# Performance work log

Hardware: AMD Instinct MI355X
Metric: run time of the kernel (lower is better)

The kernel has to match this reference:

```python
import jax, jax.numpy as jnp
import numpy as np

V, I_DIM, H_DIM, NUM_CLASSES = 32000, 300, 300, 3
B, T = 64, 128


def setup_inputs() -> dict:
    key = jax.random.key(0)
    ks = jax.random.split(key, 32)
    def g(k, shape, s=0.05):
        return (jax.random.normal(k, shape, jnp.float32) * s)
    linputs = jax.random.randint(ks[0], (B, T), 0, V)
    rinputs = jax.random.randint(ks[1], (B, T), 0, V)
    # strictly-lower-triangular binary child masks (children processed before parents)
    tril = jnp.tril(jnp.ones((T, T), jnp.float32), k=-1)
    lgraph = (jax.random.uniform(ks[2], (B, T, T)) < 0.05).astype(jnp.float32) * tril
    rgraph = (jax.random.uniform(ks[3], (B, T, T)) < 0.05).astype(jnp.float32) * tril
    emb = g(ks[4], (V, I_DIM), 0.02).at[0].set(0.0)  # padding_idx=0
    names = ['wi', 'wf', 'wo', 'wu', 'ui', 'uf', 'uo', 'uu']
    params = {}
    for n, (kw, kb) in zip(names, [(ks[5 + 2 * i], ks[6 + 2 * i]) for i in range(8)]):
        params[n + '_w'] = g(kw, (H_DIM, I_DIM if n[0] == 'w' else H_DIM))
        params[n + '_b'] = g(kb, (H_DIM,))
    params['gcn_w'] = g(ks[21], (H_DIM, H_DIM))
    params['wh_w'] = g(ks[22], (H_DIM, 4 * H_DIM))
    params['wh_b'] = g(ks[23], (H_DIM,))
    params['wp_w'] = g(ks[24], (NUM_CLASSES, H_DIM))
    params['wp_b'] = g(ks[25], (NUM_CLASSES,))
    return dict(linputs=linputs, lgraph=lgraph, rinputs=rinputs, rgraph=rgraph, emb=emb, **params)


def _lin(x, w, b):
    return x @ w.T + b


def _forward(linputs, lgraph, rinputs, rgraph, emb,
             wi_w, wi_b, wf_w, wf_b, wo_w, wo_b, wu_w, wu_b,
             ui_w, ui_b, uf_w, uf_b, uo_w, uo_b, uu_w, uu_b,
             gcn_w, wh_w, wh_b, wp_w, wp_b):
    def tree_lstm(x, graph):
        Bd, Td, _ = x.shape
        # precompute input projections for all timesteps: [B,T,H]
        Xi = _lin(x, wi_w, wi_b)
        Xf = _lin(x, wf_w, wf_b)
        Xo = _lin(x, wo_w, wo_b)
        Xu = _lin(x, wu_w, wu_b)
        h0 = jnp.zeros((Bd, Td, H_DIM), x.dtype)
        c0 = jnp.zeros_like(h0)

        def step(carry, inp):
            h, c = carry
            xi, xf, xo, xu, mrow, j = inp  # xi..xu: [B,H], mrow: [B,T]
            hj = h[:, j]  # [B,H]
            i = jax.nn.sigmoid(xi + _lin(hj, ui_w, ui_b))
            o = jax.nn.sigmoid(xo + _lin(hj, uo_w, uo_b))
            u = jnp.tanh(xu + _lin(hj, uu_w, uu_b))
            f = jax.nn.sigmoid(xf[:, None, :] + _lin(h, uf_w, uf_b))  # [B,T,H]
            c_new = i * u + jnp.einsum('bt,bth->bh', mrow, f * c)
            h_new = o * jnp.tanh(c_new)
            return (h.at[:, j].set(h_new), c.at[:, j].set(c_new)), None

        xs = (jnp.swapaxes(Xi, 0, 1), jnp.swapaxes(Xf, 0, 1),
              jnp.swapaxes(Xo, 0, 1), jnp.swapaxes(Xu, 0, 1),
              jnp.swapaxes(graph, 0, 1), jnp.arange(Td))
        (h, c), _ = jax.lax.scan(step, (h0, c0), xs)
        return h, c

    def gcn(graph, h):
        Td = graph.shape[1]
        A = jnp.eye(Td, dtype=graph.dtype)[None] + jnp.swapaxes(graph, 1, 2) + graph
        return jax.nn.relu(jnp.einsum('bst,bth->bsh', A, h @ gcn_w))

    le = emb[linputs]
    re = emb[rinputs]
    lh, _ = tree_lstm(le, lgraph)
    rh, _ = tree_lstm(re, rgraph)
    ls = gcn(lgraph, lh)
    rs = gcn(rgraph, rh)
    v = jnp.concatenate([ls.max(axis=1), rs.max(axis=1), ls.mean(axis=1), rs.mean(axis=1)], axis=1)
    return _lin(jax.nn.relu(_lin(v, wh_w, wh_b)), wp_w, wp_b)


def reference(linputs, lgraph, rinputs, rgraph, emb,
              wi_w, wi_b, wf_w, wf_b, wo_w, wo_b, wu_w, wu_b,
              ui_w, ui_b, uf_w, uf_b, uo_w, uo_b, uu_w, uu_b,
              gcn_w, wh_w, wh_b, wp_w, wp_b):
    return _forward(linputs, lgraph, rinputs, rgraph, emb,
                    wi_w, wi_b, wf_w, wf_b, wo_w, wo_b, wu_w, wu_b,
                    ui_w, ui_b, uf_w, uf_b, uo_w, uo_b, uu_w, uu_b,
                    gcn_w, wh_w, wh_b, wp_w, wp_b)
```

## Files before the change

### kernel.cpp

```cpp
#include <hip/hip_runtime.h>
#include <math.h>

#define BD 64
#define TD 128
#define HD 300
#define NROW (2*BD*TD)
#define ROWSZ ((size_t)NROW*HD)
#define CMAX 32
#define AMAX 64

__device__ __forceinline__ float sigf(float x){ return 1.f/(1.f+expf(-x)); }

__global__ __launch_bounds__(256) void gates_gemm_k(
    const int* __restrict__ tokL, const int* __restrict__ tokR,
    const float* __restrict__ emb,
    const float* __restrict__ wi_w, const float* __restrict__ wf_w,
    const float* __restrict__ wo_w, const float* __restrict__ wu_w,
    const float* __restrict__ wi_b, const float* __restrict__ ui_b,
    const float* __restrict__ wf_b, const float* __restrict__ uf_b,
    const float* __restrict__ wo_b, const float* __restrict__ uo_b,
    const float* __restrict__ wu_b, const float* __restrict__ uu_b,
    float* __restrict__ IU, float* __restrict__ Og, float* __restrict__ F0)
{
  __shared__ __align__(16) float As[32][64];
  __shared__ __align__(16) float Bs[4][32][64];
  const int r0 = blockIdx.x * 64;
  const int n0 = blockIdx.y * 64;
  const int tid = threadIdx.x;

  const int am  = tid >> 2;
  const int akq = tid & 3;
  const float* arow;
  {
    int r = r0 + am;
    int tree = r >> 13;
    int tok  = (tree ? tokR : tokL)[r & 8191];
    arow = emb + (size_t)tok * HD;
  }

  const float* Bm[4] = {wi_w, wf_w, wo_w, wu_w};
  const int bn  = tid >> 2;
  const int bkq = tid & 3;
  const bool nok = (n0 + bn) < HD;

  const int tm = tid >> 4;
  const int tn = tid & 15;
  float acc[4][4][4] = {};

  for (int k0 = 0; k0 < HD; k0 += 32){
    #pragma unroll
    for (int h = 0; h < 2; ++h){
      int k  = akq*8 + h*4;
      int kg = k0 + k;
      float4 v;
      if (kg + 3 < HD) v = *(const float4*)(arow + kg);
      else {
        v.x = (kg   < HD) ? arow[kg]   : 0.f;
        v.y = (kg+1 < HD) ? arow[kg+1] : 0.f;
        v.z = (kg+2 < HD) ? arow[kg+2] : 0.f;
        v.w = (kg+3 < HD) ? arow[kg+3] : 0.f;
      }
      As[k+0][am] = v.x; As[k+1][am] = v.y; As[k+2][am] = v.z; As[k+3][am] = v.w;
    }
    #pragma unroll
    for (int g = 0; g < 4; ++g){
      const float* brow = Bm[g] + (size_t)(n0 + bn) * HD;
      #pragma unroll
      for (int h = 0; h < 2; ++h){
        int k  = bkq*8 + h*4;
        int kg = k0 + k;
        float4 v = {0.f,0.f,0.f,0.f};
        if (nok){
          if (kg + 3 < HD) v = *(const float4*)(brow + kg);
          else {
            if (kg   < HD) v.x = brow[kg];
            if (kg+1 < HD) v.y = brow[kg+1];
            if (kg+2 < HD) v.z = brow[kg+2];
          }
        }
        Bs[g][k+0][bn] = v.x; Bs[g][k+1][bn] = v.y;
        Bs[g][k+2][bn] = v.z; Bs[g][k+3][bn] = v.w;
      }
    }
    __syncthreads();

    #pragma unroll 8
    for (int k = 0; k < 32; ++k){
      float a[4];
      *(float4*)a = *(const float4*)&As[k][tm*4];
      #pragma unroll
      for (int g = 0; g < 4; ++g){
        float bb[4];
        *(float4*)bb = *(const float4*)&Bs[g][k][tn*4];
        #pragma unroll
        for (int i = 0; i < 4; ++i)
          #pragma unroll
          for (int j = 0; j < 4; ++j)
            acc[g][i][j] += a[i]*bb[j];
      }
    }
    __syncthreads();
  }

  #pragma unroll
  for (int j = 0; j < 4; ++j){
    int col = n0 + tn*4 + j;
    if (col >= HD) continue;
    float bi = wi_b[col] + ui_b[col];
    float bf = wf_b[col] + uf_b[col];
    float bo = wo_b[col] + uo_b[col];
    float bu = wu_b[col] + uu_b[col];
    #pragma unroll
    for (int i = 0; i < 4; ++i){
      int r = r0 + tm*4 + i;
      size_t idx = (size_t)r * HD + col;
      float ii = sigf(acc[0][i][j] + bi);
      float uu = tanhf(acc[3][i][j] + bu);
      IU[idx] = ii * uu;
      Og[idx] = sigf(acc[2][i][j] + bo);
      F0[idx] = acc[1][i][j] + bf;
    }
  }
}

__global__ __launch_bounds__(256) void gemm_nn_k(
    const float* __restrict__ A, const float* __restrict__ B,
    float* __restrict__ C)
{
  __shared__ __align__(16) float As[32][64];
  __shared__ __align__(16) float Bs[32][64];
  const int r0 = blockIdx.x * 64;
  const int n0 = blockIdx.y * 64;
  const int tid = threadIdx.x;

  const int am  = tid >> 2;
  const int akq = tid & 3;
  const float* arow = A + (size_t)(r0 + am) * HD;

  const int tm = tid >> 4;
  const int tn = tid & 15;
  float acc[4][4] = {};

  for (int k0 = 0; k0 < HD; k0 += 32){
    #pragma unroll
    for (int h = 0; h < 2; ++h){
      int k  = akq*8 + h*4;
      int kg = k0 + k;
      float4 v;
      if (kg + 3 < HD) v = *(const float4*)(arow + kg);
      else {
        v.x = (kg   < HD) ? arow[kg]   : 0.f;
        v.y = (kg+1 < HD) ? arow[kg+1] : 0.f;
        v.z = (kg+2 < HD) ? arow[kg+2] : 0.f;
        v.w = (kg+3 < HD) ? arow[kg+3] : 0.f;
      }
      As[k+0][am] = v.x; As[k+1][am] = v.y; As[k+2][am] = v.z; As[k+3][am] = v.w;
    }
    {
      int bk  = tid >> 3;
      int bnq = tid & 7;
      int kg  = k0 + bk;
      const float* brow = B + (size_t)kg * HD;
      #pragma unroll
      for (int h = 0; h < 2; ++h){
        int n  = bnq*8 + h*4;
        int ng = n0 + n;
        float4 v = {0.f,0.f,0.f,0.f};
        if (kg < HD){
          if (ng + 3 < HD) v = *(const float4*)(brow + ng);
          else {
            if (ng   < HD) v.x = brow[ng];
            if (ng+1 < HD) v.y = brow[ng+1];
            if (ng+2 < HD) v.z = brow[ng+2];
          }
        }
        *(float4*)&Bs[bk][n] = v;
      }
    }
    __syncthreads();

    #pragma unroll 8
    for (int k = 0; k < 32; ++k){
      float a[4], bb[4];
      *(float4*)a  = *(const float4*)&As[k][tm*4];
      *(float4*)bb = *(const float4*)&Bs[k][tn*4];
      #pragma unroll
      for (int i = 0; i < 4; ++i)
        #pragma unroll
        for (int j = 0; j < 4; ++j)
          acc[i][j] += a[i]*bb[j];
    }
    __syncthreads();
  }

  #pragma unroll
  for (int i = 0; i < 4; ++i){
    int r = r0 + tm*4 + i;
    #pragma unroll
    for (int j = 0; j < 4; ++j){
      int col = n0 + tn*4 + j;
      if (col < HD) C[(size_t)r * HD + col] = acc[i][j];
    }
  }
}

__global__ __launch_bounds__(320) void recurrence_k(
    float* IU_C,
    float* Og_H,
    float* F0_G,
    const float* __restrict__ gL, const float* __restrict__ gR,
    const float* __restrict__ ufw)
{
  const int wg   = blockIdx.x;
  const int tree = wg >> 6;
  const int b    = wg & 63;
  const float* graph = tree ? gR : gL;
  const int tid = threadIdx.x;

  __shared__ float  cw  [TD][CMAX];
  __shared__ unsigned char cidx[TD][CMAX];
  __shared__ int    ccnt[TD];
  __shared__ int    lvl [TD];
  __shared__ int    cnt [TD+1];
  __shared__ int    cur [TD+1];
  __shared__ int    lvstart[TD+1];
  __shared__ int    order[TD];
  __shared__ int    changed, nlv_s;
  __shared__ __align__(16) float hl[32][HD];

  if (tid < TD){
    const int j = tid;
    const float* grow = graph + ((size_t)b*TD + j)*TD;
    int c = 0;
    for (int t = 0; t < j; ++t){
      float m = grow[t];
      if (m != 0.f && c < CMAX){ cidx[j][c] = (unsigned char)t; cw[j][c] = m; ++c; }
    }
    ccnt[j] = c;
    lvl[j] = 0;
  }
  __syncthreads();

  for (int it = 0; it < TD; ++it){
    if (tid == 0) changed = 0;
    __syncthreads();
    if (tid < TD){
      int m = 0, cn = ccnt[tid];
      for (int li = 0; li < cn; ++li){
        int lc = lvl[cidx[tid][li]] + 1;
        m = m > lc ? m : lc;
      }
      if (m > lvl[tid]){ lvl[tid] = m; changed = 1; }
    }
    __syncthreads();
    int ch = changed;
    __syncthreads();
    if (!ch) break;
  }

  if (tid == 0) nlv_s = 0;
  for (int q = tid; q <= TD; q += 320){ cnt[q] = 0; }
  __syncthreads();
  if (tid < TD){
    atomicMax(&nlv_s, lvl[tid] + 1);
    atomicAdd(&cnt[lvl[tid]], 1);
  }
  __syncthreads();
  const int nlv = nlv_s;
  if (tid == 0){
    int run = 0;
    for (int lv = 0; lv < nlv; ++lv){
      lvstart[lv] = run; cur[lv] = run; run += cnt[lv];
    }
    lvstart[nlv] = run;
  }
  __syncthreads();
  if (tid < TD){
    int p = atomicAdd(&cur[lvl[tid]], 1);
    order[p] = tid;
  }
  __syncthreads();

  const size_t base = (size_t)(tree*BD + b) * TD * HD;

  for (int lv = 0; lv < nlv; ++lv){
    const int s = lvstart[lv], e = lvstart[lv+1];
    const bool doB = (lv != nlv - 1);
    for (int cs0 = s; cs0 < e; cs0 += 32){
      const int csn = (e - cs0) < 32 ? (e - cs0) : 32;

      for (int q = tid; q < csn*HD; q += 320){
        int ni = q / HD;
        int d  = q - ni*HD;
        int j  = order[cs0 + ni];
        size_t rj = base + (size_t)j*HD + d;
        float f0  = F0_G[rj];
        float acc = 0.f;
        const int cn = ccnt[j];
        for (int li = 0; li < cn; ++li){
          int t = cidx[j][li];
          size_t rt = base + (size_t)t*HD + d;
          acc += cw[j][li] * sigf(f0 + F0_G[rt]) * IU_C[rt];
        }
        float c = IU_C[rj] + acc;
        float h = Og_H[rj] * tanhf(c);
        IU_C[rj] = c; Og_H[rj] = h; hl[ni][d] = h;
      }
      __syncthreads();

      if (doB){
        for (int nb0 = 0; nb0 < csn; nb0 += 8){
          if (tid < HD){
            const int d = tid;
            const float4* wrow = (const float4*)(ufw + (size_t)d * HD);
            float acc[8];
            #pragma unroll
            for (int ni = 0; ni < 8; ++ni) acc[ni] = 0.f;
            for (int k4 = 0; k4 < HD/4; ++k4){
              float4 w = wrow[k4];
              #pragma unroll
              for (int ni = 0; ni < 8; ++ni){
                float4 h4 = *(const float4*)&hl[nb0+ni][k4*4];
                acc[ni] += w.x*h4.x + w.y*h4.y + w.z*h4.z + w.w*h4.w;
              }
            }
            #pragma unroll
            for (int ni = 0; ni < 8; ++ni){
              if (nb0 + ni < csn){
                int j = order[cs0 + nb0 + ni];
                F0_G[base + (size_t)j*HD + d] = acc[ni];
              }
            }
          }
        }
      }
      __syncthreads();
    }
  }
}

__global__ __launch_bounds__(320) void gcn_pool_k(
    const float* __restrict__ HG,
    const float* __restrict__ gL, const float* __restrict__ gR,
    float* __restrict__ vbuf)
{
  const int wg   = blockIdx.x;
  const int tree = wg >> 6;
  const int b    = wg & 63;
  const float* graph = tree ? gR : gL;
  const int tid = threadIdx.x;

  __shared__ float gl[TD][TD+1];
  __shared__ float aw[TD][AMAX];
  __shared__ unsigned char ai[TD][AMAX];
  __shared__ int   acnt[TD];

  for (int q = tid; q < TD*TD; q += 320)
    gl[q >> 7][q & 127] = graph[(size_t)b*TD*TD + q];
  __syncthreads();

  if (tid < TD){
    const int s = tid;
    int c = 0;
    for (int t = 0; t < TD; ++t){
      float w = gl[s][t] + gl[t][s];
      if (w != 0.f && c < AMAX){ ai[s][c] = (unsigned char)t; aw[s][c] = w; ++c; }
    }
    acnt[s] = c;
  }
  __syncthreads();

  const size_t base = (size_t)(tree*BD + b) * TD * HD;
  if (tid < HD){
    float mx = -3.4e38f, sm = 0.f;
    for (int s = 0; s < TD; ++s){
      float v = HG[base + (size_t)s*HD + tid];
      const int cn = acnt[s];
      for (int li = 0; li < cn; ++li)
        v += aw[s][li] * HG[base + (size_t)ai[s][li]*HD + tid];
      v = fmaxf(v, 0.f);
      mx = fmaxf(mx, v);
      sm += v;
    }
    vbuf[(size_t)b*1200 + tree*HD + tid]       = mx;
    vbuf[(size_t)b*1200 + 600 + tree*HD + tid] = sm * (1.f/128.f);
  }
}

__global__ __launch_bounds__(320) void classifier_k(
    const float* __restrict__ vbuf,
    const float* __restrict__ wh_w, const float* __restrict__ wh_b,
    const float* __restrict__ wp_w, const float* __restrict__ wp_b,
    float* __restrict__ out)
{
  const int b = blockIdx.x;
  const int tid = threadIdx.x;
  __shared__ __align__(16) float vrow[1200];
  __shared__ float hid[300];
  __shared__ float red[5];

  for (int m = tid; m < 1200; m += 320) vrow[m] = vbuf[(size_t)b*1200 + m];
  __syncthreads();

  if (tid < HD){
    const float4* wrow = (const float4*)(wh_w + (size_t)tid*1200);
    float a0 = wh_b[tid], a1 = 0.f, a2 = 0.f, a3 = 0.f;
    #pragma unroll 5
    for (int m4 = 0; m4 < 300; ++m4){
      float4 w = wrow[m4];
      float4 v = *(const float4*)&vrow[m4*4];
      a0 += w.x*v.x; a1 += w.y*v.y; a2 += w.z*v.z; a3 += w.w*v.w;
    }
    hid[tid] = fmaxf((a0+a1)+(a2+a3), 0.f);
  }
  __syncthreads();

  const int wave = tid >> 6, lane = tid & 63;
  for (int n = 0; n < 3; ++n){
    float p = (tid < HD) ? wp_w[n*HD + tid] * hid[tid] : 0.f;
    #pragma unroll
    for (int off = 32; off > 0; off >>= 1) p += __shfl_down(p, off);
    if (lane == 0) red[wave] = p;
    __syncthreads();
    if (tid == 0){
      float s = wp_b[n];
      for (int wv = 0; wv < 5; ++wv) s += red[wv];
      out[(size_t)b*3 + n] = s;
    }
    __syncthreads();
  }
}

extern "C" void kernel_launch(void* const* d_in, const int* in_sizes, int n_in,
                              void* d_out, int out_size, void* d_ws, size_t ws_size,
                              hipStream_t stream) {
  const int*   linputs = (const int*)  d_in[0];
  const float* lgraph  = (const float*)d_in[1];
  const int*   rinputs = (const int*)  d_in[2];
  const float* rgraph  = (const float*)d_in[3];
  const float* emb     = (const float*)d_in[4];
  const float* wi_w = (const float*)d_in[5],  *wi_b = (const float*)d_in[6];
  const float* wf_w = (const float*)d_in[7],  *wf_b = (const float*)d_in[8];
  const float* wo_w = (const float*)d_in[9],  *wo_b = (const float*)d_in[10];
  const float* wu_w = (const float*)d_in[11], *wu_b = (const float*)d_in[12];
  const float* ui_b = (const float*)d_in[14];
  const float* uf_w = (const float*)d_in[15], *uf_b = (const float*)d_in[16];
  const float* uo_b = (const float*)d_in[18];
  const float* uu_b = (const float*)d_in[20];
  const float* gcn_w = (const float*)d_in[21];
  const float* wh_w  = (const float*)d_in[22], *wh_b = (const float*)d_in[23];
  const float* wp_w  = (const float*)d_in[24], *wp_b = (const float*)d_in[25];

  float* ws   = (float*)d_ws;
  float* buf0 = ws;
  float* buf1 = ws + 1*ROWSZ;
  float* buf2 = ws + 2*ROWSZ;
  float* vbuf = ws + 3*ROWSZ;
  float* out  = (float*)d_out;

  dim3 gg(NROW/64, 5);
  gates_gemm_k<<<gg,256,0,stream>>>(linputs, rinputs, emb,
      wi_w, wf_w, wo_w, wu_w,
      wi_b, ui_b, wf_b, uf_b, wo_b, uo_b, wu_b, uu_b,
      buf0, buf1, buf2);

  recurrence_k<<<128,320,0,stream>>>(buf0, buf1, buf2, lgraph, rgraph, uf_w);

  gemm_nn_k<<<gg,256,0,stream>>>(buf1, gcn_w, buf0);

  gcn_pool_k<<<128,320,0,stream>>>(buf0, lgraph, rgraph, vbuf);
  classifier_k<<<64,320,0,stream>>>(vbuf, wh_w, wh_b, wp_w, wp_b, out);

  (void)in_sizes; (void)n_in; (void)out_size; (void)ws_size;
}
```

Measured before the change: 1.094 ms.

## Split recurrence matvec over three K-groups with 960 threads per block

The recurrence kernel grows from 320 to 960 threads per block. The uf_w matvec is split into three 100-wide K slices whose partial sums are reduced through a new shared buffer before being written to F0_G. The child-accumulation loop is also software-pipelined so the next child's loads are issued before the current sigmoid term is computed. This adds parallelism to a latency-bound kernel that runs only 128 blocks, at the cost of an extra shared-memory reduction, an extra barrier per 8-node batch, and more register and LDS pressure.

After: 913.8 us. 1.2x faster.

```diff
diff --git a/kernel.cpp b/kernel.cpp
--- a/kernel.cpp
+++ b/kernel.cpp
@@ -8,6 +8,7 @@
 #define ROWSZ ((size_t)NROW*HD)
 #define CMAX 32
 #define AMAX 64
+#define RTHREADS 960
 
 __device__ __forceinline__ float sigf(float x){ return 1.f/(1.f+expf(-x)); }
 
@@ -204,7 +205,7 @@
   }
 }
 
-__global__ __launch_bounds__(320) void recurrence_k(
+__global__ __launch_bounds__(RTHREADS) void recurrence_k(
     float* IU_C,
     float* Og_H,
     float* F0_G,
@@ -227,6 +228,7 @@
   __shared__ int    order[TD];
   __shared__ int    changed, nlv_s;
   __shared__ __align__(16) float hl[32][HD];
+  __shared__ __align__(16) float pacc[3][8][HD];
 
   if (tid < TD){
     const int j = tid;
@@ -259,7 +261,7 @@
   }
 
   if (tid == 0) nlv_s = 0;
-  for (int q = tid; q <= TD; q += 320){ cnt[q] = 0; }
+  for (int q = tid; q <= TD; q += RTHREADS){ cnt[q] = 0; }
   __syncthreads();
   if (tid < TD){
     atomicMax(&nlv_s, lvl[tid] + 1);
@@ -283,13 +285,16 @@
 
   const size_t base = (size_t)(tree*BD + b) * TD * HD;
 
+  const int kg = tid / 320;
+  const int td = tid - kg*320;
+
   for (int lv = 0; lv < nlv; ++lv){
     const int s = lvstart[lv], e = lvstart[lv+1];
     const bool doB = (lv != nlv - 1);
     for (int cs0 = s; cs0 < e; cs0 += 32){
       const int csn = (e - cs0) < 32 ? (e - cs0) : 32;
 
-      for (int q = tid; q < csn*HD; q += 320){
+      for (int q = tid; q < csn*HD; q += RTHREADS){
         int ni = q / HD;
         int d  = q - ni*HD;
         int j  = order[cs0 + ni];
@@ -297,10 +302,20 @@
         float f0  = F0_G[rj];
         float acc = 0.f;
         const int cn = ccnt[j];
-        for (int li = 0; li < cn; ++li){
-          int t = cidx[j][li];
-          size_t rt = base + (size_t)t*HD + d;
-          acc += cw[j][li] * sigf(f0 + F0_G[rt]) * IU_C[rt];
+        if (cn > 0){
+          int   t0 = cidx[j][0];
+          float w0 = cw[j][0];
+          float g0 = F0_G[base + (size_t)t0*HD + d];
+          float c0 = IU_C[base + (size_t)t0*HD + d];
+          for (int li = 1; li < cn; ++li){
+            int   t1 = cidx[j][li];
+            float w1 = cw[j][li];
+            float g1 = F0_G[base + (size_t)t1*HD + d];
+            float c1 = IU_C[base + (size_t)t1*HD + d];
+            acc += w0 * sigf(f0 + g0) * c0;
+            w0 = w1; g0 = g1; c0 = c1;
+          }
+          acc += w0 * sigf(f0 + g0) * c0;
         }
         float c = IU_C[rj] + acc;
         float h = Og_H[rj] * tanhf(c);
@@ -310,31 +325,40 @@
 
       if (doB){
         for (int nb0 = 0; nb0 < csn; nb0 += 8){
-          if (tid < HD){
-            const int d = tid;
-            const float4* wrow = (const float4*)(ufw + (size_t)d * HD);
+          if (td < HD){
+            const int d = td;
+            const float4* wrow = (const float4*)(ufw + (size_t)d * HD) + kg*25;
             float acc[8];
             #pragma unroll
             for (int ni = 0; ni < 8; ++ni) acc[ni] = 0.f;
-            for (int k4 = 0; k4 < HD/4; ++k4){
+            #pragma unroll 5
+            for (int k4 = 0; k4 < 25; ++k4){
               float4 w = wrow[k4];
+              const int kb = kg*100 + k4*4;
               #pragma unroll
               for (int ni = 0; ni < 8; ++ni){
-                float4 h4 = *(const float4*)&hl[nb0+ni][k4*4];
+                float4 h4 = *(const float4*)&hl[nb0+ni][kb];
                 acc[ni] += w.x*h4.x + w.y*h4.y + w.z*h4.z + w.w*h4.w;
               }
             }
             #pragma unroll
-            for (int ni = 0; ni < 8; ++ni){
-              if (nb0 + ni < csn){
-                int j = order[cs0 + nb0 + ni];
-                F0_G[base + (size_t)j*HD + d] = acc[ni];
-              }
+            for (int ni = 0; ni < 8; ++ni) pacc[kg][ni][d] = acc[ni];
+          }
+          __syncthreads();
+          for (int q = tid; q < 8*HD; q += RTHREADS){
+            int ni = q / HD;
+            int d  = q - ni*HD;
+            if (nb0 + ni < csn){
+              int j = order[cs0 + nb0 + ni];
+              F0_G[base + (size_t)j*HD + d] =
+                  pacc[0][ni][d] + pacc[1][ni][d] + pacc[2][ni][d];
             }
           }
+          __syncthreads();
         }
-      }
-      __syncthreads();
+      } else {
+        __syncthreads();
+      }
     }
   }
 }
@@ -464,7 +488,7 @@
       wi_b, ui_b, wf_b, uf_b, wo_b, uo_b, wu_b, uu_b,
       buf0, buf1, buf2);
 
-  recurrence_k<<<128,320,0,stream>>>(buf0, buf1, buf2, lgraph, rgraph, uf_w);
+  recurrence_k<<<128,RTHREADS,0,stream>>>(buf0, buf1, buf2, lgraph, rgraph, uf_w);
 
   gemm_nn_k<<<gg,256,0,stream>>>(buf1, gcn_w, buf0);
 
```
